# Optimization experiments

Hardware: AMD Instinct MI355X
Metric: run time of the kernel (lower is better)

Reference implementation:

```python
import jax, jax.numpy as jnp
import numpy as np

NH = 8       # num_heads
EDIM = 256   # embedding_dim (also per-head dim in this module)
BS, SQL = 4, 1024


def setup_inputs() -> dict:
    key = jax.random.key(0)
    ks = jax.random.split(key, 5)
    scale_in = 1.0 / np.sqrt(EDIM)
    scale_out = 1.0 / np.sqrt(NH * EDIM)
    return {
        "x": jax.random.normal(ks[0], (BS, SQL, EDIM), dtype=jnp.float32),
        "w_attn": jax.random.normal(ks[1], (NH * 3 * EDIM, EDIM), dtype=jnp.float32) * scale_in,
        "b_attn": jax.random.normal(ks[2], (NH * 3 * EDIM,), dtype=jnp.float32) * scale_in,
        "w_out": jax.random.normal(ks[3], (EDIM, NH * EDIM), dtype=jnp.float32) * scale_out,
        "b_out": jax.random.normal(ks[4], (EDIM,), dtype=jnp.float32) * scale_out,
    }


def reference(x, w_attn, b_attn, w_out, b_out):
    bs, sql, edim = x.shape
    nh = NH
    # projections: (bs, sql, nh*3*edim); split into Q, K, V chunks of nh*edim
    proj = x @ w_attn.T + b_attn
    q, k, v = jnp.split(proj, 3, axis=-1)
    # Faithful to torch: raw view (bs, sql, nh*edim) -> (bs, nh, sql, edim),
    # a reinterpretation of memory, NOT a transpose.
    q = q.reshape(bs, nh, sql, edim)
    k = k.reshape(bs, nh, sql, edim)
    v = v.reshape(bs, nh, sql, edim)
    # scaled dot-product scores: (bs, nh, sql, sql)
    scores = jnp.einsum("bhqd,bhkd->bhqk", q, k) / jnp.sqrt(jnp.float32(edim))
    # causal mask: -inf strictly above the diagonal (equivalent to adding triu(-inf, 1))
    causal = jnp.tril(jnp.ones((sql, sql), dtype=bool))
    scores = jnp.where(causal, scores, -jnp.inf)
    attn = jax.nn.softmax(scores, axis=-1)
    out = jnp.einsum("bhqk,bhkd->bhqd", attn, v)
    # Faithful raw view back: (bs, nh, sql, edim) -> (bs, sql, nh*edim)
    out = out.reshape(bs, sql, nh * edim)
    return out @ w_out.T + b_out
```

## Files before the change

### kernel.cpp

```cpp
#include <hip/hip_runtime.h>

#define SQL  1024
#define EDIM 256
#define NHD  8
#define NKV  (NHD * 3 * EDIM)
#define MROWS (4 * SQL)

typedef short bf16x8 __attribute__((ext_vector_type(8)));
typedef float f32x4 __attribute__((ext_vector_type(4)));

__device__ __forceinline__ unsigned short f2bf(float f) {
  unsigned u = __float_as_uint(f);
  u += 0x7fff + ((u >> 16) & 1);
  return (unsigned short)(u >> 16);
}
__device__ __forceinline__ float bf2f(unsigned short s) {
  return __uint_as_float(((unsigned)s) << 16);
}

__device__ __forceinline__ void g2lds16(const void* g, void* l) {
  __builtin_amdgcn_global_load_lds(
      (const __attribute__((address_space(1))) unsigned int*)g,
      (__attribute__((address_space(3))) unsigned int*)l, 16, 0, 0);
}

__device__ __forceinline__ void storev(float* p, float v) { *p = v; }
__device__ __forceinline__ void storev(unsigned short* p, float v) { *p = f2bf(v); }

__global__ __launch_bounds__(256) void cast3_bf16(
    const float* __restrict__ x, unsigned short* __restrict__ xb,
    const float* __restrict__ wa, unsigned short* __restrict__ wb,
    const float* __restrict__ wo, unsigned short* __restrict__ wob) {
  const float* src; unsigned short* dst; int i;
  int blk = blockIdx.x;
  if (blk < 512)       { src = x;  dst = xb;  i = blk * 256 + threadIdx.x; }
  else if (blk < 1280) { src = wa; dst = wb;  i = (blk - 512) * 256 + threadIdx.x; }
  else                 { src = wo; dst = wob; i = (blk - 1280) * 256 + threadIdx.x; }
  float4 a = ((const float4*)src)[2 * i];
  float4 b = ((const float4*)src)[2 * i + 1];
  union { unsigned short s[8]; ulonglong2 v; } u;
  u.s[0] = f2bf(a.x); u.s[1] = f2bf(a.y); u.s[2] = f2bf(a.z); u.s[3] = f2bf(a.w);
  u.s[4] = f2bf(b.x); u.s[5] = f2bf(b.y); u.s[6] = f2bf(b.z); u.s[7] = f2bf(b.w);
  ((ulonglong2*)dst)[i] = u.v;
}

template <int BM, int BN, typename OutT>
__global__ __launch_bounds__(256) void gemm_mfma(
    const unsigned short* __restrict__ A, const unsigned short* __restrict__ B,
    const float* __restrict__ bias, OutT* __restrict__ C,
    int M, int N, int K) {
  constexpr int TM = BM / 32, TN = BN / 32;
  __shared__ __align__(16) unsigned short As[2][BM * 32];
  __shared__ __align__(16) unsigned short Bs[2][BN * 32];
  const int tid = threadIdx.x;
  const int wave = tid >> 6, lane = tid & 63;
  const int quad = lane >> 4, l16 = lane & 15;
  const int wm = (wave >> 1) * (BM / 2), wn = (wave & 1) * (BN / 2);
  const int m0 = blockIdx.x * BM, n0 = blockIdx.y * BN;
  const int sw = (l16 >> 1) & 3;

  f32x4 acc[TM][TN];
  #pragma unroll
  for (int i = 0; i < TM; i++)
    #pragma unroll
    for (int j = 0; j < TN; j++) acc[i][j] = {0.f, 0.f, 0.f, 0.f};

  auto stage = [&](int k0, int bb) {
    #pragma unroll
    for (int it = 0; it < BM / 64; it++) {
      int flat = it * 256 + tid;
      int row = flat >> 2;
      int cg = (flat & 3) ^ ((row >> 1) & 3);
      g2lds16(A + (size_t)(m0 + row) * K + k0 + cg * 8, &As[bb][flat * 8]);
    }
    #pragma unroll
    for (int it = 0; it < BN / 64; it++) {
      int flat = it * 256 + tid;
      int row = flat >> 2;
      int cg = (flat & 3) ^ ((row >> 1) & 3);
      g2lds16(B + (size_t)(n0 + row) * K + k0 + cg * 8, &Bs[bb][flat * 8]);
    }
  };

  stage(0, 0);
  __syncthreads();
  for (int k0 = 0; k0 < K; k0 += 32) {
    const int bb = (k0 >> 5) & 1;
    if (k0 + 32 < K) stage(k0 + 32, bb ^ 1);
    bf16x8 af[TM], bf[TN];
    #pragma unroll
    for (int i = 0; i < TM; i++)
      af[i] = *(const bf16x8*)&As[bb][(wm + i * 16 + l16) * 32 + (quad ^ sw) * 8];
    #pragma unroll
    for (int j = 0; j < TN; j++)
      bf[j] = *(const bf16x8*)&Bs[bb][(wn + j * 16 + l16) * 32 + (quad ^ sw) * 8];
    #pragma unroll
    for (int i = 0; i < TM; i++)
      #pragma unroll
      for (int j = 0; j < TN; j++)
        acc[i][j] = __builtin_amdgcn_mfma_f32_16x16x32_bf16(af[i], bf[j], acc[i][j], 0, 0, 0);
    __syncthreads();
  }

  #pragma unroll
  for (int i = 0; i < TM; i++) {
    #pragma unroll
    for (int r = 0; r < 4; r++) {
      int m = m0 + wm + i * 16 + quad * 4 + r;
      #pragma unroll
      for (int j = 0; j < TN; j++) {
        int n = n0 + wn + j * 16 + l16;
        storev(&C[(size_t)m * N + n], acc[i][j][r] + bias[n]);
      }
    }
  }
}

__global__ __launch_bounds__(256) void transpose_v(
    const unsigned short* __restrict__ proj, unsigned short* __restrict__ vt) {
  __shared__ unsigned short T[64][66];
  const int tid = threadIdx.x;
  const int s0 = blockIdx.x * 64, d0 = blockIdx.y * 64, bh = blockIdx.z;
  const int b = bh >> 3, h = bh & 7;
  #pragma unroll
  for (int it = 0; it < 2; it++) {
    int c = it * 256 + tid;
    int sr = c >> 3, k8 = (c & 7) * 8;
    int s = s0 + sr;
    const unsigned short* src = proj + (size_t)(b * SQL + h * 128 + (s >> 3)) * NKV
                                + 2 * 2048 + (s & 7) * 256 + d0 + k8;
    *(ulonglong2*)&T[sr][k8] = *(const ulonglong2*)src;
  }
  __syncthreads();
  #pragma unroll
  for (int it = 0; it < 2; it++) {
    int c = it * 256 + tid;
    int dr = c >> 3, s8 = (c & 7) * 8;
    unsigned short tmp[8];
    #pragma unroll
    for (int j = 0; j < 8; j++) tmp[j] = T[s8 + j][dr];
    unsigned short* dst = vt + ((size_t)bh * EDIM + d0 + dr) * SQL + s0 + s8;
    *(ulonglong2*)dst = *(ulonglong2*)tmp;
  }
}

__global__ __launch_bounds__(256) void attn_mfma(
    const unsigned short* __restrict__ proj,
    const unsigned short* __restrict__ vt,
    unsigned short* __restrict__ opart,
    float* __restrict__ lpart) {
  __shared__ __align__(16) unsigned short lds[37888];

  const int tid = threadIdx.x;
  const int wave = tid >> 6, lane = tid & 63;
  const int quad = lane >> 4, l16 = lane & 15;
  unsigned short* Ps = lds + 32768 + wave * 1280;

  const int g = blockIdx.x;
  const int bh = g & 31;
  const int rem = g >> 5;
  const int j = rem & 3;
  const int sb = rem >> 2;
  const int b = bh >> 3, h = bh & 7;
  const int t0 = 4 * (8 - j);
  const int m0cnt = (j < 2) ? 4 : 3;
  const int s1st  = (j < 2) ? 3 : 2;
  const int lo = 9 * sb, hi = lo + 9;

  int segqt[2], segk0[2], seglen[2], segr[2];
  int nseg = 0;
  if (lo < t0) {
    int e = (hi < t0) ? hi : t0;
    segqt[nseg] = 7 - j; segk0[nseg] = lo; seglen[nseg] = e - lo;
    segr[nseg] = sb; nseg++;
  }
  if (hi > t0) {
    int a = (lo > t0) ? lo : t0;
    segqt[nseg] = j; segk0[nseg] = a - t0; seglen[nseg] = hi - a;
    segr[nseg] = m0cnt + (sb - s1st); nseg++;
  }

  auto stage = [&](int kt, int bb) {
    unsigned short* KsB = lds + bb * 8192;
    unsigned short* VtB = lds + 16384 + bb * 8192;
    #pragma unroll
    for (int it = 0; it < 4; it++) {
      int flat = it * 256 + tid;
      int row = flat >> 5, ch = (flat & 31) ^ (row & 7);
      int s = kt * 32 + row;
      g2lds16(proj + (size_t)(b * SQL + h * 128 + (s >> 3)) * NKV + 2048
                   + (s & 7) * 256 + ch * 8,
              KsB + flat * 8);
    }
    #pragma unroll
    for (int it = 0; it < 4; it++) {
      int flat = it * 256 + tid;
      int d = flat >> 2, ch = (flat & 3) ^ ((d >> 1) & 3);
      g2lds16(vt + ((size_t)bh * EDIM + d) * SQL + kt * 32 + ch * 8,
              VtB + flat * 8);
    }
  };

  for (int sg = 0; sg < nseg; sg++) {
    const int qt = segqt[sg];
    const int q0 = qt * 128;
    const int c0 = segk0[sg], len = seglen[sg];

    bf16x8 aq[2][8];
    #pragma unroll
    for (int st = 0; st < 2; st++) {
      int s = q0 + wave * 32 + st * 16 + l16;
      const unsigned short* qrow =
          proj + (size_t)(b * SQL + h * 128 + (s >> 3)) * NKV + (s & 7) * 256;
      #pragma unroll
      for (int kk = 0; kk < 8; kk++)
        aq[st][kk] = *(const bf16x8*)(qrow + kk * 32 + quad * 8);
    }

    f32x4 o[2][16];
    #pragma unroll
    for (int st = 0; st < 2; st++)
      #pragma unroll
      for (int tt = 0; tt < 16; tt++) o[st][tt] = {0.f, 0.f, 0.f, 0.f};
    float l_r[2][4] = {};

    stage(c0, 0);
    __syncthreads();

    for (int i = 0; i < len; i++) {
      const int kt = c0 + i;
      const int bb = i & 1;
      if (i + 1 < len) stage(kt + 1, bb ^ 1);
      const unsigned short* KsB = lds + bb * 8192;
      const unsigned short* VtB = lds + 16384 + bb * 8192;

      f32x4 s[2][2];
      #pragma unroll
      for (int st = 0; st < 2; st++)
        #pragma unroll
        for (int c = 0; c < 2; c++) s[st][c] = {0.f, 0.f, 0.f, 0.f};
      #pragma unroll
      for (int c = 0; c < 2; c++) {
        #pragma unroll
        for (int kk = 0; kk < 8; kk++) {
          int ch = (kk * 4 + quad) ^ (l16 & 7);
          bf16x8 bk = *(const bf16x8*)&KsB[(c * 16 + l16) * 256 + ch * 8];
          s[0][c] = __builtin_amdgcn_mfma_f32_16x16x32_bf16(aq[0][kk], bk, s[0][c], 0, 0, 0);
          s[1][c] = __builtin_amdgcn_mfma_f32_16x16x32_bf16(aq[1][kk], bk, s[1][c], 0, 0, 0);
        }
      }

      #pragma unroll
      for (int st = 0; st < 2; st++) {
        #pragma unroll
        for (int c = 0; c < 2; c++) {
          int kg = kt * 32 + c * 16 + l16;
          #pragma unroll
          for (int r = 0; r < 4; r++) {
            int qg = q0 + wave * 32 + st * 16 + quad * 4 + r;
            float p = (kg <= qg) ? __expf(s[st][c][r] * 0.0625f) : 0.f;
            l_r[st][r] += p;
            Ps[(st * 16 + quad * 4 + r) * 40 + c * 16 + l16] = f2bf(p);
          }
        }
      }

      bf16x8 ap0 = *(const bf16x8*)&Ps[l16 * 40 + quad * 8];
      bf16x8 ap1 = *(const bf16x8*)&Ps[(16 + l16) * 40 + quad * 8];
      #pragma unroll
      for (int tt = 0; tt < 16; tt++) {
        int ch = quad ^ ((l16 >> 1) & 3);
        bf16x8 bv = *(const bf16x8*)&VtB[(tt * 16 + l16) * 32 + ch * 8];
        o[0][tt] = __builtin_amdgcn_mfma_f32_16x16x32_bf16(ap0, bv, o[0][tt], 0, 0, 0);
        o[1][tt] = __builtin_amdgcn_mfma_f32_16x16x32_bf16(ap1, bv, o[1][tt], 0, 0, 0);
      }
      __syncthreads();
    }

    const int slot = (bh * 4 + j) * 5 + segr[sg];
    #pragma unroll
    for (int st = 0; st < 2; st++) {
      #pragma unroll
      for (int r = 0; r < 4; r++) {
        float l = l_r[st][r];
        #pragma unroll
        for (int off = 1; off < 16; off <<= 1) l += __shfl_xor(l, off);
        float inv = (l > 0.f) ? 1.0f / l : 0.f;
        int sl = wave * 32 + st * 16 + quad * 4 + r;
        if (l16 == 0) lpart[slot * 128 + sl] = l;
        unsigned short* dst = opart + (size_t)slot * 32768 + sl * 256;
        #pragma unroll
        for (int tt = 0; tt < 16; tt++)
          dst[tt * 16 + l16] = f2bf(o[st][tt][r] * inv);
      }
    }
  }
}

__global__ __launch_bounds__(256) void combine_split(
    const unsigned short* __restrict__ opart, const float* __restrict__ lpart,
    unsigned short* __restrict__ obf) {
  int idx = blockIdx.x * 256 + threadIdx.x;
  int row = idx >> 5, oct = idx & 31;
  int bh = row >> 10, s = row & 1023;
  int qt = s >> 7, sl = s & 127;
  int j, r0, rn;
  if (qt >= 4) {
    j = 7 - qt; r0 = 0; rn = (j < 2) ? 4 : 3;
  } else {
    j = qt; int m0 = (j < 2) ? 4 : 3; r0 = m0; rn = 5 - m0;
  }
  int base = (bh * 4 + j) * 5;
  float acc[8] = {};
  float L = 0.f;
  for (int r = r0; r < r0 + rn; r++) {
    int slot = base + r;
    float l = lpart[slot * 128 + sl];
    L += l;
    union { unsigned short s[8]; ulonglong2 v; } u;
    u.v = *(const ulonglong2*)(opart + (size_t)slot * 32768 + sl * 256 + oct * 8);
    #pragma unroll
    for (int k = 0; k < 8; k++) acc[k] += bf2f(u.s[k]) * l;
  }
  float w = 1.0f / L;
  union { unsigned short s[8]; ulonglong2 v; } uo;
  #pragma unroll
  for (int k = 0; k < 8; k++) uo.s[k] = f2bf(acc[k] * w);
  int b = bh >> 3, h = bh & 7;
  unsigned short* dst = obf + (size_t)(b * SQL + h * 128 + (s >> 3)) * 2048
                        + (s & 7) * 256 + oct * 8;
  *(ulonglong2*)dst = uo.v;
}

extern "C" void kernel_launch(void* const* d_in, const int* in_sizes, int n_in,
                              void* d_out, int out_size, void* d_ws, size_t ws_size,
                              hipStream_t stream) {
  const float* x      = (const float*)d_in[0];
  const float* w_attn = (const float*)d_in[1];
  const float* b_attn = (const float*)d_in[2];
  const float* w_out  = (const float*)d_in[3];
  const float* b_out  = (const float*)d_in[4];
  float* out = (float*)d_out;

  char* p = (char*)d_ws;
  unsigned short* proj  = (unsigned short*)p;  p += (size_t)MROWS * NKV * 2;
  unsigned short* vtb   = (unsigned short*)p;  p += (size_t)32 * EDIM * SQL * 2;
  unsigned short* xb    = (unsigned short*)p;  p += (size_t)MROWS * EDIM * 2;
  unsigned short* wb    = (unsigned short*)p;  p += (size_t)NKV * EDIM * 2;
  unsigned short* wob   = (unsigned short*)p;  p += (size_t)EDIM * 2048 * 2;
  unsigned short* opart = (unsigned short*)p;  p += (size_t)640 * 32768 * 2;
  float*          lpart = (float*)p;
  unsigned short* obf   = vtb;

  cast3_bf16<<<1536, 256, 0, stream>>>(x, xb, w_attn, wb, w_out, wob);
  gemm_mfma<128, 128, unsigned short><<<dim3(MROWS / 128, NKV / 128), 256, 0, stream>>>(
      xb, wb, b_attn, proj, MROWS, NKV, EDIM);
  transpose_v<<<dim3(SQL / 64, EDIM / 64, 32), 256, 0, stream>>>(proj, vtb);
  attn_mfma<<<512, 256, 0, stream>>>(proj, vtb, opart, lpart);
  combine_split<<<4096, 256, 0, stream>>>(opart, lpart, obf);
  gemm_mfma<64, 64, float><<<dim3(MROWS / 64, EDIM / 64), 256, 0, stream>>>(
      obf, wob, b_out, out, MROWS, EDIM, NHD * EDIM);
}
```

Baseline: 189.1 us.

## Split attention block across 8 waves with 16 query rows per wave

The attention kernel now launches 512 threads (8 waves) per block instead of 256, and each wave owns 16 query rows rather than 32. This halves the per-wave accumulator and Q-fragment register footprint and adds a launch-bounds hint asking for more resident blocks, aiming to raise occupancy and latency hiding. The trade-off is that each K fragment loaded from LDS now feeds fewer MFMAs, which lowers reuse and increases LDS read traffic per FLOP.

```diff
diff --git a/kernel.cpp b/kernel.cpp
--- a/kernel.cpp
+++ b/kernel.cpp
@@ -144,7 +144,7 @@
   }
 }
 
-__global__ __launch_bounds__(256) void attn_mfma(
+__global__ __launch_bounds__(512, 4) void attn_mfma(
     const unsigned short* __restrict__ proj,
     const unsigned short* __restrict__ vt,
     unsigned short* __restrict__ opart,
@@ -154,7 +154,7 @@
   const int tid = threadIdx.x;
   const int wave = tid >> 6, lane = tid & 63;
   const int quad = lane >> 4, l16 = lane & 15;
-  unsigned short* Ps = lds + 32768 + wave * 1280;
+  unsigned short* Ps = lds + 32768 + wave * 640;
 
   const int g = blockIdx.x;
   const int bh = g & 31;
@@ -184,8 +184,8 @@
     unsigned short* KsB = lds + bb * 8192;
     unsigned short* VtB = lds + 16384 + bb * 8192;
     #pragma unroll
-    for (int it = 0; it < 4; it++) {
-      int flat = it * 256 + tid;
+    for (int it = 0; it < 2; it++) {
+      int flat = it * 512 + tid;
       int row = flat >> 5, ch = (flat & 31) ^ (row & 7);
       int s = kt * 32 + row;
       g2lds16(proj + (size_t)(b * SQL + h * 128 + (s >> 3)) * NKV + 2048
@@ -193,8 +193,8 @@
               KsB + flat * 8);
     }
     #pragma unroll
-    for (int it = 0; it < 4; it++) {
-      int flat = it * 256 + tid;
+    for (int it = 0; it < 2; it++) {
+      int flat = it * 512 + tid;
       int d = flat >> 2, ch = (flat & 3) ^ ((d >> 1) & 3);
       g2lds16(vt + ((size_t)bh * EDIM + d) * SQL + kt * 32 + ch * 8,
               VtB + flat * 8);
@@ -206,23 +206,20 @@
     const int q0 = qt * 128;
     const int c0 = segk0[sg], len = seglen[sg];
 
-    bf16x8 aq[2][8];
-    #pragma unroll
-    for (int st = 0; st < 2; st++) {
-      int s = q0 + wave * 32 + st * 16 + l16;
+    bf16x8 aq[8];
+    {
+      int s = q0 + wave * 16 + l16;
       const unsigned short* qrow =
           proj + (size_t)(b * SQL + h * 128 + (s >> 3)) * NKV + (s & 7) * 256;
       #pragma unroll
       for (int kk = 0; kk < 8; kk++)
-        aq[st][kk] = *(const bf16x8*)(qrow + kk * 32 + quad * 8);
-    }
-
-    f32x4 o[2][16];
-    #pragma unroll
-    for (int st = 0; st < 2; st++)
-      #pragma unroll
-      for (int tt = 0; tt < 16; tt++) o[st][tt] = {0.f, 0.f, 0.f, 0.f};
-    float l_r[2][4] = {};
+        aq[kk] = *(const bf16x8*)(qrow + kk * 32 + quad * 8);
+    }
+
+    f32x4 o[16];
+    #pragma unroll
+    for (int tt = 0; tt < 16; tt++) o[tt] = {0.f, 0.f, 0.f, 0.f};
+    float l_r[4] = {};
 
     stage(c0, 0);
     __syncthreads();
@@ -234,65 +231,50 @@
       const unsigned short* KsB = lds + bb * 8192;
       const unsigned short* VtB = lds + 16384 + bb * 8192;
 
-      f32x4 s[2][2];
-      #pragma unroll
-      for (int st = 0; st < 2; st++)
-        #pragma unroll
-        for (int c = 0; c < 2; c++) s[st][c] = {0.f, 0.f, 0.f, 0.f};
-      #pragma unroll
-      for (int c = 0; c < 2; c++) {
-        #pragma unroll
-        for (int kk = 0; kk < 8; kk++) {
-          int ch = (kk * 4 + quad) ^ (l16 & 7);
-          bf16x8 bk = *(const bf16x8*)&KsB[(c * 16 + l16) * 256 + ch * 8];
-          s[0][c] = __builtin_amdgcn_mfma_f32_16x16x32_bf16(aq[0][kk], bk, s[0][c], 0, 0, 0);
-          s[1][c] = __builtin_amdgcn_mfma_f32_16x16x32_bf16(aq[1][kk], bk, s[1][c], 0, 0, 0);
-        }
+      f32x4 s0 = {0.f, 0.f, 0.f, 0.f}, s1 = {0.f, 0.f, 0.f, 0.f};
+      #pragma unroll
+      for (int kk = 0; kk < 8; kk++) {
+        int ch = (kk * 4 + quad) ^ (l16 & 7);
+        bf16x8 b0 = *(const bf16x8*)&KsB[l16 * 256 + ch * 8];
+        bf16x8 b1 = *(const bf16x8*)&KsB[(16 + l16) * 256 + ch * 8];
+        s0 = __builtin_amdgcn_mfma_f32_16x16x32_bf16(aq[kk], b0, s0, 0, 0, 0);
+        s1 = __builtin_amdgcn_mfma_f32_16x16x32_bf16(aq[kk], b1, s1, 0, 0, 0);
       }
 
-      #pragma unroll
-      for (int st = 0; st < 2; st++) {
-        #pragma unroll
-        for (int c = 0; c < 2; c++) {
-          int kg = kt * 32 + c * 16 + l16;
-          #pragma unroll
-          for (int r = 0; r < 4; r++) {
-            int qg = q0 + wave * 32 + st * 16 + quad * 4 + r;
-            float p = (kg <= qg) ? __expf(s[st][c][r] * 0.0625f) : 0.f;
-            l_r[st][r] += p;
-            Ps[(st * 16 + quad * 4 + r) * 40 + c * 16 + l16] = f2bf(p);
-          }
-        }
+      const int kg0 = kt * 32 + l16, kg1 = kg0 + 16;
+      #pragma unroll
+      for (int r = 0; r < 4; r++) {
+        int qg = q0 + wave * 16 + quad * 4 + r;
+        float p0 = (kg0 <= qg) ? __expf(s0[r] * 0.0625f) : 0.f;
+        float p1 = (kg1 <= qg) ? __expf(s1[r] * 0.0625f) : 0.f;
+        l_r[r] += p0 + p1;
+        Ps[(quad * 4 + r) * 40 + l16]      = f2bf(p0);
+        Ps[(quad * 4 + r) * 40 + 16 + l16] = f2bf(p1);
       }
 
-      bf16x8 ap0 = *(const bf16x8*)&Ps[l16 * 40 + quad * 8];
-      bf16x8 ap1 = *(const bf16x8*)&Ps[(16 + l16) * 40 + quad * 8];
+      bf16x8 ap = *(const bf16x8*)&Ps[l16 * 40 + quad * 8];
       #pragma unroll
       for (int tt = 0; tt < 16; tt++) {
         int ch = quad ^ ((l16 >> 1) & 3);
         bf16x8 bv = *(const bf16x8*)&VtB[(tt * 16 + l16) * 32 + ch * 8];
-        o[0][tt] = __builtin_amdgcn_mfma_f32_16x16x32_bf16(ap0, bv, o[0][tt], 0, 0, 0);
-        o[1][tt] = __builtin_amdgcn_mfma_f32_16x16x32_bf16(ap1, bv, o[1][tt], 0, 0, 0);
+        o[tt] = __builtin_amdgcn_mfma_f32_16x16x32_bf16(ap, bv, o[tt], 0, 0, 0);
       }
       __syncthreads();
     }
 
     const int slot = (bh * 4 + j) * 5 + segr[sg];
     #pragma unroll
-    for (int st = 0; st < 2; st++) {
-      #pragma unroll
-      for (int r = 0; r < 4; r++) {
-        float l = l_r[st][r];
-        #pragma unroll
-        for (int off = 1; off < 16; off <<= 1) l += __shfl_xor(l, off);
-        float inv = (l > 0.f) ? 1.0f / l : 0.f;
-        int sl = wave * 32 + st * 16 + quad * 4 + r;
-        if (l16 == 0) lpart[slot * 128 + sl] = l;
-        unsigned short* dst = opart + (size_t)slot * 32768 + sl * 256;
-        #pragma unroll
-        for (int tt = 0; tt < 16; tt++)
-          dst[tt * 16 + l16] = f2bf(o[st][tt][r] * inv);
-      }
+    for (int r = 0; r < 4; r++) {
+      float l = l_r[r];
+      #pragma unroll
+      for (int off = 1; off < 16; off <<= 1) l += __shfl_xor(l, off);
+      float inv = (l > 0.f) ? 1.0f / l : 0.f;
+      int sl = wave * 16 + quad * 4 + r;
+      if (l16 == 0) lpart[slot * 128 + sl] = l;
+      unsigned short* dst = opart + (size_t)slot * 32768 + sl * 256;
+      #pragma unroll
+      for (int tt = 0; tt < 16; tt++)
+        dst[tt * 16 + l16] = f2bf(o[tt][r] * inv);
     }
   }
 }
@@ -356,7 +338,7 @@
   gemm_mfma<128, 128, unsigned short><<<dim3(MROWS / 128, NKV / 128), 256, 0, stream>>>(
       xb, wb, b_attn, proj, MROWS, NKV, EDIM);
   transpose_v<<<dim3(SQL / 64, EDIM / 64, 32), 256, 0, stream>>>(proj, vtb);
-  attn_mfma<<<512, 256, 0, stream>>>(proj, vtb, opart, lpart);
+  attn_mfma<<<512, 512, 0, stream>>>(proj, vtb, opart, lpart);
   combine_split<<<4096, 256, 0, stream>>>(opart, lpart, obf);
   gemm_mfma<64, 64, float><<<dim3(MROWS / 64, EDIM / 64), 256, 0, stream>>>(
       obf, wob, b_out, out, MROWS, EDIM, NHD * EDIM);
```

Measured after the change: 233.5 us. 1.23x slower.
